# Performance work log

Measured on AMD Instinct MI355X. Metric: run time of the kernel, lower is better.

Reference implementation:

```python
import jax, jax.numpy as jnp
import numpy as np

N_NODES = 50000
C = 128
E = 800000
B = 4096
NEG = 5
NUM_LAYERS = 3


def setup_inputs() -> dict:
    key = jax.random.key(0)
    ks = jax.random.split(key, 8)
    edge_index = jax.random.randint(ks[0], (2, E), 0, N_NODES, dtype=jnp.int64)
    edge_weight = jax.random.uniform(ks[1], (E,), dtype=jnp.float32)
    n_id = jax.random.randint(ks[2], ((2 + NEG) * B,), 0, N_NODES, dtype=jnp.int64)
    x = jnp.zeros((1,), jnp.float32)  # ignored by forward (overwritten by id_embed)
    id_embed = jax.random.normal(ks[3], (N_NODES, C), jnp.float32) * 0.1
    w1 = jax.random.normal(ks[4], (2 * C, C), jnp.float32) * (1.0 / np.sqrt(2 * C))
    b1 = jnp.zeros((C,), jnp.float32)
    w2 = jax.random.normal(ks[5], (C, 1), jnp.float32) * (1.0 / np.sqrt(C))
    b2 = jnp.zeros((1,), jnp.float32)
    return {"x": x, "edge_index": edge_index, "edge_weight": edge_weight,
            "n_id": n_id, "neg_sample_num": NEG, "id_embed": id_embed,
            "w1": w1, "b1": b1, "w2": w2, "b2": b2}


def reference(x, edge_index, edge_weight, n_id, neg_sample_num, id_embed, w1, b1, w2, b2):
    n_nodes = id_embed.shape[0]
    row, col = edge_index[0], edge_index[1]
    # symmetric GCN normalization (LGCConv)
    deg = jax.ops.segment_sum(jnp.ones_like(row, dtype=id_embed.dtype), row,
                              num_segments=n_nodes)
    dinv = jnp.where(deg > 0, jax.lax.rsqrt(jnp.maximum(deg, 1e-12)), 0.0)
    norm = (dinv[row] * dinv[col])[:, None]  # [E,1]
    h = id_embed
    final = id_embed
    for _ in range(NUM_LAYERS):
        h = jax.ops.segment_sum(norm * h[col], row, num_segments=n_nodes)
        final = final + h
    final = final / (NUM_LAYERS + 1)
    # split n_id into (out, pos, neg) index groups
    b = n_id.shape[0] // (2 + neg_sample_num)
    out = final[n_id[:b]]
    pos = final[n_id[b:2 * b]]
    neg = final[n_id[2 * b:]]
    tiled_out = jnp.repeat(out, neg_sample_num, axis=0)  # [b*neg, C]

    def pred_head(z):  # Linear -> LeakyReLU(0.2) -> (Dropout eval=identity) -> Linear
        z = jax.nn.leaky_relu(z @ w1 + b1, negative_slope=0.2)
        return z @ w2 + b2

    pos_logit = pred_head(jnp.concatenate([out, pos], axis=-1))
    neg_logits = pred_head(jnp.concatenate([tiled_out, neg], axis=-1))
    return pos_logit, neg_logits
```

## Files before the change

kernel.cpp:

```cpp
#include <hip/hip_runtime.h>
#include <hip/hip_bf16.h>

#define C 128
#define NBKT 128
#define BCAP 8192

typedef __bf16 bf16x8 __attribute__((ext_vector_type(8)));
typedef float floatx4 __attribute__((ext_vector_type(4)));

__device__ __forceinline__ unsigned short f2bf(float f) {
    unsigned u = __float_as_uint(f);
    unsigned r = (u + 0x7FFFu + ((u >> 16) & 1u)) >> 16;
    return (unsigned short)r;
}
__device__ __forceinline__ float bflo(unsigned v) { return __uint_as_float(v << 16); }
__device__ __forceinline__ float bfhi(unsigned v) { return __uint_as_float(v & 0xFFFF0000u); }
__device__ __forceinline__ unsigned packbf(float lo, float hi) {
    return (unsigned)f2bf(lo) | ((unsigned)f2bf(hi) << 16);
}

__device__ __forceinline__ int g_idx(const void* p, long long i, int is64) {
    if (is64) return (int)((const long long*)p)[i];
    return ((const int*)p)[i];
}
__device__ __forceinline__ float g_flt(const void* p, long long i, int isf32) {
    if (isf32) return ((const float*)p)[i];
    return __uint_as_float(((unsigned)((const unsigned short*)p)[i]) << 16);
}

__global__ void k_detect(const void* edge, const void* nid, const void* emb, int* flags,
                         unsigned* g0, unsigned* g1, unsigned* g2, int* bucketcnt,
                         int N, int SST) {
    int t = threadIdx.x;
    int buf = t >> 6, w = t & 63;
    size_t o = (size_t)(w >> 5) * SST + (size_t)N * 32 + (w & 31);
    if (buf == 0) g0[o] = 0;
    else if (buf == 1) g1[o] = 0;
    else g2[o] = 0;
    if (t < NBKT) bucketcnt[t] = 0;
    if (t < 64) {
        const unsigned* wrd = (const unsigned*)edge;
        const unsigned* nw = (const unsigned*)nid;
        int predA = (t < 32) ? (wrd[2 * t + 1] == 0u) : 1;
        int predB = (t < 32) ? (nw[2 * t + 1] == 0u) : 1;
        const unsigned short* h = (const unsigned short*)emb;
        int ex = (h[2 * t] >> 7) & 0xFF;
        int plaus = (ex >= 0x6C && ex <= 0x7F) ? 1 : 0;
        unsigned long long mA = __ballot(predA);
        unsigned long long mB = __ballot(predB);
        unsigned long long mP = __ballot(plaus);
        if (t == 0) {
            flags[0] = (mA == ~0ull) ? 1 : 0;
            flags[1] = (mB == ~0ull) ? 1 : 0;
            flags[2] = (__popcll(mP) < 32) ? 1 : 0;
        }
    }
}

__global__ void k_bucketA(const void* edge, int E, int rpb, const int* flags,
                          unsigned* __restrict__ bucketbuf, int* __restrict__ bucketcnt) {
    __shared__ int lcnt[NBKT];
    __shared__ int lbase[NBKT];
    int t = threadIdx.x;
    int is64 = flags[0];
    const int PER = 8;
    int chunkSz = blockDim.x * PER;
    long long stride = (long long)gridDim.x * chunkSz;
    for (long long base = (long long)blockIdx.x * chunkSz; base < E; base += stride) {
        if (t < NBKT) lcnt[t] = 0;
        __syncthreads();
        int bkt[PER], rank[PER];
        unsigned enc[PER];
        long long e0 = base + (long long)t * PER;
        int rr[PER], cc[PER];
        if (e0 + PER <= E) {
            if (is64) {
                const long long* pr = (const long long*)edge + e0;
                const long long* pc = (const long long*)edge + E + e0;
#pragma unroll
                for (int j = 0; j < PER; j += 2) {
                    longlong2 vr = *(const longlong2*)(pr + j);
                    longlong2 vc = *(const longlong2*)(pc + j);
                    rr[j] = (int)vr.x; rr[j + 1] = (int)vr.y;
                    cc[j] = (int)vc.x; cc[j + 1] = (int)vc.y;
                }
            } else {
                const int* pr = (const int*)edge + e0;
                const int* pc = (const int*)edge + E + e0;
#pragma unroll
                for (int j = 0; j < PER; j += 4) {
                    int4 vr = *(const int4*)(pr + j);
                    int4 vc = *(const int4*)(pc + j);
                    rr[j] = vr.x; rr[j + 1] = vr.y; rr[j + 2] = vr.z; rr[j + 3] = vr.w;
                    cc[j] = vc.x; cc[j + 1] = vc.y; cc[j + 2] = vc.z; cc[j + 3] = vc.w;
                }
            }
#pragma unroll
            for (int j = 0; j < PER; ++j) {
                int b = rr[j] / rpb;
                bkt[j] = b;
                enc[j] = ((unsigned)(rr[j] - b * rpb) << 16) | (unsigned)(cc[j] & 0xFFFF);
                rank[j] = atomicAdd(&lcnt[b], 1);
            }
        } else {
#pragma unroll
            for (int j = 0; j < PER; ++j) {
                long long e = e0 + j;
                if (e < E) {
                    int r = g_idx(edge, e, is64);
                    int c = g_idx(edge, (long long)E + e, is64);
                    int b = r / rpb;
                    bkt[j] = b;
                    enc[j] = ((unsigned)(r - b * rpb) << 16) | (unsigned)(c & 0xFFFF);
                    rank[j] = atomicAdd(&lcnt[b], 1);
                } else bkt[j] = -1;
            }
        }
        __syncthreads();
        if (t < NBKT) lbase[t] = atomicAdd(&bucketcnt[t], lcnt[t]);
        __syncthreads();
#pragma unroll
        for (int j = 0; j < PER; ++j) {
            if (bkt[j] >= 0) {
                int pos = lbase[bkt[j]] + rank[j];
                if (pos < BCAP)
                    bucketbuf[(size_t)bkt[j] * BCAP + pos] = enc[j];
            }
        }
    }
}

__global__ __launch_bounds__(512) void k_bsort(
        const unsigned* __restrict__ bucketbuf, const int* __restrict__ bucketcnt,
        int* __restrict__ rowptr, float* __restrict__ dinv, float* __restrict__ di2,
        float* __restrict__ rdinv, unsigned short* __restrict__ cols16, int N, int rpb) {
    __shared__ int hist[512];
    int b = blockIdx.x;
    int t = threadIdx.x;
    int base = 0, cnt = 0, total = 0;
    for (int i = 0; i < NBKT; ++i) {
        int v = bucketcnt[i];
        if (v > BCAP) v = BCAP;
        if (i < b) base += v;
        if (i == b) cnt = v;
        total += v;
    }
    int r0 = b * rpb;
    int rows = N - r0;
    if (rows > rpb) rows = rpb;
    if (rows < 0) rows = 0;

    hist[t] = 0;
    __syncthreads();
    const unsigned* buf = bucketbuf + (size_t)b * BCAP;
    for (int i = t; i < cnt; i += 512) atomicAdd(&hist[buf[i] >> 16], 1);
    __syncthreads();
    int v = hist[t];
    __syncthreads();
    for (int off = 1; off < 512; off <<= 1) {
        int x = (t >= off) ? hist[t - off] : 0;
        __syncthreads();
        hist[t] += x;
        __syncthreads();
    }
    int excl = hist[t] - v;
    if (t < rows) {
        int r = r0 + t;
        rowptr[r] = base + excl;
        float fd = (float)v;
        float dv = (v > 0) ? rsqrtf(fd) : 0.0f;
        dinv[r] = dv;
        di2[r] = dv * dv;
        rdinv[r] = (v > 0) ? sqrtf(fd) : 0.0f;
    }
    if (b == NBKT - 1 && t == 0) rowptr[N] = total;
    __syncthreads();
    hist[t] = base + excl;
    __syncthreads();
    for (int i = t; i < cnt; i += 512) {
        unsigned u = buf[i];
        int pos = atomicAdd(&hist[u >> 16], 1);
        cols16[pos] = (unsigned short)(u & 0xFFFF);
    }
}

__global__ void k_initprep(const void* emb, const float* __restrict__ dinv,
                           unsigned* __restrict__ h0, unsigned* __restrict__ g0,
                           int n2, int SST,
                           const void* w1, const void* b1, const void* w2, const void* b2,
                           unsigned short* __restrict__ w1t, float* __restrict__ b1f,
                           float* __restrict__ w2f, float* __restrict__ b2f, const int* flags) {
    int i = blockIdx.x * blockDim.x + threadIdx.x;
    int f32 = flags[2];
    if (i < n2) {
        float lo = g_flt(emb, 2LL * i, f32);
        float hi = g_flt(emb, 2LL * i + 1, f32);
        int n = i >> 6, w = i & 63;
        size_t o = (size_t)(w >> 5) * SST + (size_t)n * 32 + (w & 31);
        h0[o] = packbf(lo, hi);
        float dv = dinv[n];
        g0[o] = packbf(lo * dv, hi * dv);
    }
    if (i < 256 * 128) {
        int k = i >> 7, n = i & 127;
        w1t[n * 256 + k] = f2bf(g_flt(w1, i, f32));
    }
    if (i < 128) {
        b1f[i] = g_flt(b1, i, f32);
        w2f[i] = g_flt(w2, i, f32);
    }
    if (i == 0) b2f[0] = g_flt(b2, 0, f32);
}

__global__ void k_layer(const int* __restrict__ rowptr, const unsigned short* __restrict__ cols16,
                        const uint4* __restrict__ gin, uint4* __restrict__ gout,
                        const float* __restrict__ di2, int N, int SSTU4) {
    int b = blockIdx.x;
    int slice = (b >> 2) & 1;
    int tile = ((b >> 3) << 2) | (b & 3);
    int node = tile * 32 + (threadIdx.x >> 3);
    if (node >= N) return;
    int l8 = threadIdx.x & 7;
    const uint4* gs = gin + (size_t)slice * SSTU4;
    int p = rowptr[node];
    int end = rowptr[node + 1];
    float a0 = 0.f, a1 = 0.f, a2 = 0.f, a3 = 0.f;
    float a4 = 0.f, a5 = 0.f, a6 = 0.f, a7 = 0.f;
    for (int base = p; base < end; base += 8) {
        int c[8];
#pragma unroll
        for (int j = 0; j < 8; ++j) {
            int idx = base + j;
            int cv = cols16[idx];
            c[j] = (idx < end) ? cv : N;
        }
#pragma unroll
        for (int j = 0; j < 8; ++j) {
            uint4 v = gs[(size_t)c[j] * 8 + l8];
            a0 += bflo(v.x); a1 += bfhi(v.x);
            a2 += bflo(v.y); a3 += bfhi(v.y);
            a4 += bflo(v.z); a5 += bfhi(v.z);
            a6 += bflo(v.w); a7 += bfhi(v.w);
        }
    }
    float s = di2[node];
    uint4 o;
    o.x = packbf(a0 * s, a1 * s);
    o.y = packbf(a2 * s, a3 * s);
    o.z = packbf(a4 * s, a5 * s);
    o.w = packbf(a6 * s, a7 * s);
    gout[(size_t)slice * SSTU4 + (size_t)node * 8 + l8] = o;
}

__global__ void k_layer3(const int* __restrict__ rowptr, const unsigned short* __restrict__ cols16,
                         const uint4* __restrict__ gin , const uint4* __restrict__ h0,
                         const uint4* __restrict__ g1, uint4* __restrict__ fin,
                         const float* __restrict__ di2, const float* __restrict__ rdinv,
                         int N, int SSTU4) {
    int b = blockIdx.x;
    int slice = (b >> 2) & 1;
    int tile = ((b >> 3) << 2) | (b & 3);
    int node = tile * 32 + (threadIdx.x >> 3);
    if (node >= N) return;
    int l8 = threadIdx.x & 7;
    size_t sb = (size_t)slice * SSTU4;
    const uint4* gs = gin + sb;
    int p = rowptr[node];
    int end = rowptr[node + 1];
    float a0 = 0.f, a1 = 0.f, a2 = 0.f, a3 = 0.f;
    float a4 = 0.f, a5 = 0.f, a6 = 0.f, a7 = 0.f;
    for (int base = p; base < end; base += 8) {
        int c[8];
#pragma unroll
        for (int j = 0; j < 8; ++j) {
            int idx = base + j;
            int cv = cols16[idx];
            c[j] = (idx < end) ? cv : N;
        }
#pragma unroll
        for (int j = 0; j < 8; ++j) {
            uint4 v = gs[(size_t)c[j] * 8 + l8];
            a0 += bflo(v.x); a1 += bfhi(v.x);
            a2 += bflo(v.y); a3 += bfhi(v.y);
            a4 += bflo(v.z); a5 += bfhi(v.z);
            a6 += bflo(v.w); a7 += bfhi(v.w);
        }
    }
    float s = di2[node];
    float rd = rdinv[node];
    size_t ro = (size_t)node * 8 + l8;
    uint4 x0 = h0[sb + ro];
    uint4 x1 = g1[sb + ro];
    uint4 x2 = gs[ro];
    uint4 o;
    o.x = packbf(0.25f * (bflo(x0.x) + rd * (bflo(x1.x) + bflo(x2.x) + s * a0)),
                 0.25f * (bfhi(x0.x) + rd * (bfhi(x1.x) + bfhi(x2.x) + s * a1)));
    o.y = packbf(0.25f * (bflo(x0.y) + rd * (bflo(x1.y) + bflo(x2.y) + s * a2)),
                 0.25f * (bfhi(x0.y) + rd * (bfhi(x1.y) + bfhi(x2.y) + s * a3)));
    o.z = packbf(0.25f * (bflo(x0.z) + rd * (bflo(x1.z) + bflo(x2.z) + s * a4)),
                 0.25f * (bfhi(x0.z) + rd * (bfhi(x1.z) + bfhi(x2.z) + s * a5)));
    o.w = packbf(0.25f * (bflo(x0.w) + rd * (bflo(x1.w) + bflo(x2.w) + s * a6)),
                 0.25f * (bfhi(x0.w) + rd * (bfhi(x1.w) + bfhi(x2.w) + s * a7)));
    fin[(size_t)node * 16 + slice * 8 + l8] = o;
}

__global__ void k_head(const uint4* __restrict__ fin, const void* n_id,
                       const unsigned short* __restrict__ w1t,
                       const float* __restrict__ b1f, const float* __restrict__ w2f,
                       const float* __restrict__ b2f,
                       float* __restrict__ out, int B, int NEG, const int* flags) {
    __shared__ unsigned short z[64][264];
    int t = threadIdx.x;
    int id64 = flags[1];
    int mbase = blockIdx.x * 64;

#pragma unroll
    for (int i = 0; i < 8; ++i) {
        int flat = i * 256 + t;
        int m = flat >> 5;
        int q = flat & 31;
        int gm = mbase + m;
        int r;
        if (gm < B) {
            r = (q < 16) ? g_idx(n_id, gm, id64) : g_idx(n_id, B + gm, id64);
        } else {
            int j = gm - B;
            r = (q < 16) ? g_idx(n_id, j / NEG, id64) : g_idx(n_id, 2 * B + j, id64);
        }
        uint4 v = fin[(size_t)r * 16 + (q & 15)];
        *(uint4*)((char*)&z[m][0] + q * 16) = v;
    }
    __syncthreads();

    int wave = t >> 6, lane = t & 63;
    int quad = lane >> 4, l16 = lane & 15;

    floatx4 acc[8] = {};
    bf16x8 a[8];
    const unsigned short* zrow = &z[wave * 16 + l16][0];
#pragma unroll
    for (int ks = 0; ks < 8; ++ks)
        a[ks] = *(const bf16x8*)(zrow + ks * 32 + quad * 8);

#pragma unroll
    for (int ks = 0; ks < 8; ++ks) {
#pragma unroll
        for (int nt = 0; nt < 8; ++nt) {
            bf16x8 b = *(const bf16x8*)(w1t + (nt * 16 + l16) * 256 + ks * 32 + quad * 8);
            acc[nt] = __builtin_amdgcn_mfma_f32_16x16x32_bf16(a[ks], b, acc[nt], 0, 0, 0);
        }
    }

    float s0 = 0.f, s1 = 0.f, s2 = 0.f, s3 = 0.f;
#pragma unroll
    for (int nt = 0; nt < 8; ++nt) {
        int col = nt * 16 + l16;
        float bb = b1f[col], ww = w2f[col];
        float v0 = acc[nt][0] + bb; v0 = (v0 > 0.f) ? v0 : 0.2f * v0; s0 += v0 * ww;
        float v1 = acc[nt][1] + bb; v1 = (v1 > 0.f) ? v1 : 0.2f * v1; s1 += v1 * ww;
        float v2 = acc[nt][2] + bb; v2 = (v2 > 0.f) ? v2 : 0.2f * v2; s2 += v2 * ww;
        float v3 = acc[nt][3] + bb; v3 = (v3 > 0.f) ? v3 : 0.2f * v3; s3 += v3 * ww;
    }
#pragma unroll
    for (int off = 1; off <= 8; off <<= 1) {
        s0 += __shfl_xor(s0, off, 64);
        s1 += __shfl_xor(s1, off, 64);
        s2 += __shfl_xor(s2, off, 64);
        s3 += __shfl_xor(s3, off, 64);
    }
    if (l16 == 0) {
        int rowbase = mbase + wave * 16 + quad * 4;
        float bb2 = b2f[0];
        out[rowbase + 0] = s0 + bb2;
        out[rowbase + 1] = s1 + bb2;
        out[rowbase + 2] = s2 + bb2;
        out[rowbase + 3] = s3 + bb2;
    }
}

extern "C" void kernel_launch(void* const* d_in, const int* in_sizes, int n_in,
                              void* d_out, int out_size, void* d_ws, size_t ws_size,
                              hipStream_t stream) {
    const void* edge_index = d_in[1];
    const void* n_id       = d_in[3];
    const void* id_embed   = d_in[5];
    const void* w1 = d_in[6];
    const void* b1 = d_in[7];
    const void* w2 = d_in[8];
    const void* b2 = d_in[9];
    float* out = (float*)d_out;

    const int E  = in_sizes[1] / 2;
    const int N  = in_sizes[5] / C;
    const int NEG = 5;
    const int B  = in_sizes[3] / (2 + NEG);
    const int n_out_rows = B + B * NEG;
    const int SST = (N + 1) * 32;
    const int SSTU4 = (N + 1) * 8;
    const int NB = 2 * SST;
    const int rpb = (N + NBKT - 1) / NBKT;

    size_t off = 0;
    auto alloc = [&](size_t nf) {
        char* p = (char*)d_ws + off * 4;
        off += (nf + 255) & ~(size_t)255;
        return p;
    };
    int*   flags     = (int*)alloc(8);
    int*   bucketcnt = (int*)alloc(NBKT);
    float* dinv      = (float*)alloc(N);
    float* di2       = (float*)alloc(N);
    float* rdinv     = (float*)alloc(N);
    int*   rowptr    = (int*)alloc(N + 1);
    unsigned short* cols16 = (unsigned short*)alloc(((size_t)E + 16 + 1) / 2);
    unsigned* bucketbuf = (unsigned*)alloc((size_t)NBKT * BCAP);
    unsigned* h0     = (unsigned*)alloc(NB);
    unsigned* g0     = (unsigned*)alloc(NB);
    unsigned* g1     = (unsigned*)alloc(NB);
    unsigned* g2     = (unsigned*)alloc(NB);
    unsigned* fin    = (unsigned*)alloc((size_t)N * 64);
    unsigned short* w1t = (unsigned short*)alloc(256 * 128 / 2);
    float* b1f       = (float*)alloc(C);
    float* w2f       = (float*)alloc(C);
    float* b2f       = (float*)alloc(8);

    const int BS = 256;
    k_detect<<<1, 192, 0, stream>>>(edge_index, n_id, id_embed, flags, g0, g1, g2,
                                    bucketcnt, N, SST);
    const int gridA = (E + BS * 8 - 1) / (BS * 8);
    k_bucketA<<<gridA, BS, 0, stream>>>(edge_index, E, rpb, flags, bucketbuf, bucketcnt);
    k_bsort<<<NBKT, 512, 0, stream>>>(bucketbuf, bucketcnt, rowptr, dinv, di2, rdinv,
                                      cols16, N, rpb);
    k_initprep<<<(N * 64 + BS - 1) / BS, BS, 0, stream>>>(
        id_embed, dinv, h0, g0, N * 64, SST, w1, b1, w2, b2, w1t, b1f, w2f, b2f, flags);

    const int tiles = (N + 31) / 32;
    const int layer_grid = 8 * ((tiles + 3) / 4);
    k_layer<<<layer_grid, BS, 0, stream>>>(rowptr, cols16, (const uint4*)g0, (uint4*)g1,
                                           di2, N, SSTU4);
    k_layer<<<layer_grid, BS, 0, stream>>>(rowptr, cols16, (const uint4*)g1, (uint4*)g2,
                                           di2, N, SSTU4);
    k_layer3<<<layer_grid, BS, 0, stream>>>(rowptr, cols16, (const uint4*)g2, (const uint4*)h0,
                                            (const uint4*)g1, (uint4*)fin, di2, rdinv,
                                            N, SSTU4);

    k_head<<<n_out_rows / 64, BS, 0, stream>>>((const uint4*)fin, n_id, w1t, b1f, w2f, b2f,
                                               out, B, NEG, flags);
}
```

Measured before the change: 215.5 us.

## Fold detect kernel into consumers and drop g0 prescaled buffer

```diff
diff --git a/kernel.cpp b/kernel.cpp
--- a/kernel.cpp
+++ b/kernel.cpp
@@ -28,41 +28,20 @@
     return __uint_as_float(((unsigned)((const unsigned short*)p)[i]) << 16);
 }
 
-__global__ void k_detect(const void* edge, const void* nid, const void* emb, int* flags,
-                         unsigned* g0, unsigned* g1, unsigned* g2, int* bucketcnt,
-                         int N, int SST) {
-    int t = threadIdx.x;
-    int buf = t >> 6, w = t & 63;
-    size_t o = (size_t)(w >> 5) * SST + (size_t)N * 32 + (w & 31);
-    if (buf == 0) g0[o] = 0;
-    else if (buf == 1) g1[o] = 0;
-    else g2[o] = 0;
-    if (t < NBKT) bucketcnt[t] = 0;
-    if (t < 64) {
-        const unsigned* wrd = (const unsigned*)edge;
-        const unsigned* nw = (const unsigned*)nid;
-        int predA = (t < 32) ? (wrd[2 * t + 1] == 0u) : 1;
-        int predB = (t < 32) ? (nw[2 * t + 1] == 0u) : 1;
-        const unsigned short* h = (const unsigned short*)emb;
-        int ex = (h[2 * t] >> 7) & 0xFF;
-        int plaus = (ex >= 0x6C && ex <= 0x7F) ? 1 : 0;
-        unsigned long long mA = __ballot(predA);
-        unsigned long long mB = __ballot(predB);
-        unsigned long long mP = __ballot(plaus);
-        if (t == 0) {
-            flags[0] = (mA == ~0ull) ? 1 : 0;
-            flags[1] = (mB == ~0ull) ? 1 : 0;
-            flags[2] = (__popcll(mP) < 32) ? 1 : 0;
-        }
-    }
-}
-
-__global__ void k_bucketA(const void* edge, int E, int rpb, const int* flags,
+__global__ void k_bucketA(const void* edge, int E, int rpb,
                           unsigned* __restrict__ bucketbuf, int* __restrict__ bucketcnt) {
     __shared__ int lcnt[NBKT];
     __shared__ int lbase[NBKT];
+    __shared__ int sflag;
     int t = threadIdx.x;
-    int is64 = flags[0];
+    if (t < 64) {
+        const unsigned* wrd = (const unsigned*)edge;
+        int predA = (t < 32) ? (wrd[2 * t + 1] == 0u) : 1;
+        unsigned long long mA = __ballot(predA);
+        if (t == 0) sflag = (mA == ~0ull) ? 1 : 0;
+    }
+    __syncthreads();
+    int is64 = sflag;
     const int PER = 8;
     int chunkSz = blockDim.x * PER;
     long long stride = (long long)gridDim.x * chunkSz;
@@ -173,7 +152,10 @@
         di2[r] = dv * dv;
         rdinv[r] = (v > 0) ? sqrtf(fd) : 0.0f;
     }
-    if (b == NBKT - 1 && t == 0) rowptr[N] = total;
+    if (b == NBKT - 1 && t == 0) {
+        rowptr[N] = total;
+        dinv[N] = 0.f;
+    }
     __syncthreads();
     hist[t] = base + excl;
     __syncthreads();
@@ -184,22 +166,29 @@
     }
 }
 
-__global__ void k_initprep(const void* emb, const float* __restrict__ dinv,
-                           unsigned* __restrict__ h0, unsigned* __restrict__ g0,
-                           int n2, int SST,
+__global__ void k_initprep(const void* emb,
+                           unsigned* __restrict__ h0, unsigned* __restrict__ g1,
+                           unsigned* __restrict__ g2, int n2, int SST,
                            const void* w1, const void* b1, const void* w2, const void* b2,
                            unsigned short* __restrict__ w1t, float* __restrict__ b1f,
-                           float* __restrict__ w2f, float* __restrict__ b2f, const int* flags) {
-    int i = blockIdx.x * blockDim.x + threadIdx.x;
-    int f32 = flags[2];
+                           float* __restrict__ w2f, float* __restrict__ b2f) {
+    __shared__ int sf32;
+    int t = threadIdx.x;
+    if (t < 64) {
+        const unsigned short* h = (const unsigned short*)emb;
+        int ex = (h[2 * t] >> 7) & 0xFF;
+        unsigned long long mP = __ballot(ex >= 0x6C && ex <= 0x7F);
+        if (t == 0) sf32 = (__popcll(mP) < 32) ? 1 : 0;
+    }
+    __syncthreads();
+    int f32 = sf32;
+    int i = blockIdx.x * blockDim.x + t;
     if (i < n2) {
         float lo = g_flt(emb, 2LL * i, f32);
         float hi = g_flt(emb, 2LL * i + 1, f32);
         int n = i >> 6, w = i & 63;
         size_t o = (size_t)(w >> 5) * SST + (size_t)n * 32 + (w & 31);
         h0[o] = packbf(lo, hi);
-        float dv = dinv[n];
-        g0[o] = packbf(lo * dv, hi * dv);
     }
     if (i < 256 * 128) {
         int k = i >> 7, n = i & 127;
@@ -210,11 +199,18 @@
         w2f[i] = g_flt(w2, i, f32);
     }
     if (i == 0) b2f[0] = g_flt(b2, 0, f32);
-}
-
-__global__ void k_layer(const int* __restrict__ rowptr, const unsigned short* __restrict__ cols16,
-                        const uint4* __restrict__ gin, uint4* __restrict__ gout,
-                        const float* __restrict__ di2, int N, int SSTU4) {
+    if (i < 64) {
+        int s = i >> 5, w = i & 31;
+        size_t o = (size_t)s * SST + (size_t)(n2 >> 6) * 32 + w;
+        h0[o] = 0u; g1[o] = 0u; g2[o] = 0u;
+    }
+}
+
+template<bool SC>
+__global__ void k_layer_t(const int* __restrict__ rowptr, const unsigned short* __restrict__ cols16,
+                          const uint4* __restrict__ gin, uint4* __restrict__ gout,
+                          const float* __restrict__ dsc, const float* __restrict__ di2,
+                          int N, int SSTU4) {
     int b = blockIdx.x;
     int slice = (b >> 2) & 1;
     int tile = ((b >> 3) << 2) | (b & 3);
@@ -237,10 +233,18 @@
 #pragma unroll
         for (int j = 0; j < 8; ++j) {
             uint4 v = gs[(size_t)c[j] * 8 + l8];
-            a0 += bflo(v.x); a1 += bfhi(v.x);
-            a2 += bflo(v.y); a3 += bfhi(v.y);
-            a4 += bflo(v.z); a5 += bfhi(v.z);
-            a6 += bflo(v.w); a7 += bfhi(v.w);
+            if (SC) {
+                float dc = dsc[c[j]];
+                a0 = fmaf(dc, bflo(v.x), a0); a1 = fmaf(dc, bfhi(v.x), a1);
+                a2 = fmaf(dc, bflo(v.y), a2); a3 = fmaf(dc, bfhi(v.y), a3);
+                a4 = fmaf(dc, bflo(v.z), a4); a5 = fmaf(dc, bfhi(v.z), a5);
+                a6 = fmaf(dc, bflo(v.w), a6); a7 = fmaf(dc, bfhi(v.w), a7);
+            } else {
+                a0 += bflo(v.x); a1 += bfhi(v.x);
+                a2 += bflo(v.y); a3 += bfhi(v.y);
+                a4 += bflo(v.z); a5 += bfhi(v.z);
+                a6 += bflo(v.w); a7 += bfhi(v.w);
+            }
         }
     }
     float s = di2[node];
@@ -308,10 +312,18 @@
                        const unsigned short* __restrict__ w1t,
                        const float* __restrict__ b1f, const float* __restrict__ w2f,
                        const float* __restrict__ b2f,
-                       float* __restrict__ out, int B, int NEG, const int* flags) {
+                       float* __restrict__ out, int B, int NEG) {
     __shared__ unsigned short z[64][264];
+    __shared__ int sid;
     int t = threadIdx.x;
-    int id64 = flags[1];
+    if (t < 64) {
+        const unsigned* nw = (const unsigned*)n_id;
+        int predB = (t < 32) ? (nw[2 * t + 1] == 0u) : 1;
+        unsigned long long mB = __ballot(predB);
+        if (t == 0) sid = (mB == ~0ull) ? 1 : 0;
+    }
+    __syncthreads();
+    int id64 = sid;
     int mbase = blockIdx.x * 64;
 
 #pragma unroll
@@ -406,16 +418,14 @@
         off += (nf + 255) & ~(size_t)255;
         return p;
     };
-    int*   flags     = (int*)alloc(8);
     int*   bucketcnt = (int*)alloc(NBKT);
-    float* dinv      = (float*)alloc(N);
+    float* dinv      = (float*)alloc(N + 1);
     float* di2       = (float*)alloc(N);
     float* rdinv     = (float*)alloc(N);
     int*   rowptr    = (int*)alloc(N + 1);
     unsigned short* cols16 = (unsigned short*)alloc(((size_t)E + 16 + 1) / 2);
     unsigned* bucketbuf = (unsigned*)alloc((size_t)NBKT * BCAP);
     unsigned* h0     = (unsigned*)alloc(NB);
-    unsigned* g0     = (unsigned*)alloc(NB);
     unsigned* g1     = (unsigned*)alloc(NB);
     unsigned* g2     = (unsigned*)alloc(NB);
     unsigned* fin    = (unsigned*)alloc((size_t)N * 64);
@@ -425,25 +435,25 @@
     float* b2f       = (float*)alloc(8);
 
     const int BS = 256;
-    k_detect<<<1, 192, 0, stream>>>(edge_index, n_id, id_embed, flags, g0, g1, g2,
-                                    bucketcnt, N, SST);
+    hipMemsetAsync(bucketcnt, 0, NBKT * sizeof(int), stream);
+
     const int gridA = (E + BS * 8 - 1) / (BS * 8);
-    k_bucketA<<<gridA, BS, 0, stream>>>(edge_index, E, rpb, flags, bucketbuf, bucketcnt);
+    k_bucketA<<<gridA, BS, 0, stream>>>(edge_index, E, rpb, bucketbuf, bucketcnt);
     k_bsort<<<NBKT, 512, 0, stream>>>(bucketbuf, bucketcnt, rowptr, dinv, di2, rdinv,
                                       cols16, N, rpb);
     k_initprep<<<(N * 64 + BS - 1) / BS, BS, 0, stream>>>(
-        id_embed, dinv, h0, g0, N * 64, SST, w1, b1, w2, b2, w1t, b1f, w2f, b2f, flags);
+        id_embed, h0, g1, g2, N * 64, SST, w1, b1, w2, b2, w1t, b1f, w2f, b2f);
 
     const int tiles = (N + 31) / 32;
     const int layer_grid = 8 * ((tiles + 3) / 4);
-    k_layer<<<layer_grid, BS, 0, stream>>>(rowptr, cols16, (const uint4*)g0, (uint4*)g1,
-                                           di2, N, SSTU4);
-    k_layer<<<layer_grid, BS, 0, stream>>>(rowptr, cols16, (const uint4*)g1, (uint4*)g2,
-                                           di2, N, SSTU4);
+    k_layer_t<true><<<layer_grid, BS, 0, stream>>>(rowptr, cols16, (const uint4*)h0,
+                                                   (uint4*)g1, dinv, di2, N, SSTU4);
+    k_layer_t<false><<<layer_grid, BS, 0, stream>>>(rowptr, cols16, (const uint4*)g1,
+                                                    (uint4*)g2, nullptr, di2, N, SSTU4);
     k_layer3<<<layer_grid, BS, 0, stream>>>(rowptr, cols16, (const uint4*)g2, (const uint4*)h0,
                                             (const uint4*)g1, (uint4*)fin, di2, rdinv,
                                             N, SSTU4);
 
     k_head<<<n_out_rows / 64, BS, 0, stream>>>((const uint4*)fin, n_id, w1t, b1f, w2f, b2f,
-                                               out, B, NEG, flags);
-}
+                                               out, B, NEG);
+}
```

Result: slower. 221.7 us (+2.9%).
